# Kernel tuning notes

Hardware: AMD Instinct MI355X
Metric: run time of the kernel (lower is better)

The kernel has to match this reference:

```python
import jax, jax.numpy as jnp
import numpy as np

B, S, W = 64, 128, 20
VOCAB, E, H = 256, 64, 256


def setup_inputs() -> dict:
    key = jax.random.key(0)
    ks = jax.random.split(key, 10)
    return {
        "chars": jax.random.randint(ks[0], (B, S, W), 0, VOCAB),
        "emb": jax.random.uniform(ks[1], (VOCAB, E), jnp.float32, -0.32, 0.32),
        "w1": jax.random.normal(ks[2], (H, E, 1), jnp.float32) * 0.1,
        "b1": jax.random.normal(ks[3], (H,), jnp.float32) * 0.1,
        "w3": jax.random.normal(ks[4], (H, E, 3), jnp.float32) * 0.1,
        "b3": jax.random.normal(ks[5], (H,), jnp.float32) * 0.1,
        "w5": jax.random.normal(ks[6], (H, E, 5), jnp.float32) * 0.1,
        "b5": jax.random.normal(ks[7], (H,), jnp.float32) * 0.1,
        "lw": jax.random.normal(ks[8], (H, 3 * H), jnp.float32) * 0.05,
        "lb": jax.random.normal(ks[9], (H,), jnp.float32) * 0.05,
    }


def _conv_relu_maxpool(x, w, b):
    # x: [N, E, W], w: [H, E, k] ('same' padding k//2) -> [N, H]
    k = w.shape[-1]
    pad = k // 2
    y = jax.lax.conv_general_dilated(
        x, w, window_strides=(1,), padding=[(pad, pad)],
        dimension_numbers=("NCH", "OIH", "NCH"))
    y = jax.nn.relu(y + b[None, :, None])
    return jnp.max(y, axis=2)  # global max over char positions


def reference(chars, emb, w1, b1, w3, b3, w5, b5, lw, lb):
    b, s, wlen = chars.shape
    flat = chars.reshape(-1, wlen)                 # [N, W]
    x = emb[flat]                                  # [N, W, E]
    x = jnp.transpose(x, (0, 2, 1))                # [N, E, W]
    outs = jnp.concatenate([
        _conv_relu_maxpool(x, w1, b1),
        _conv_relu_maxpool(x, w3, b3),
        _conv_relu_maxpool(x, w5, b5),
    ], axis=1)                                     # [N, 3H]
    out = outs @ lw.T + lb                         # [N, H]
    return out.reshape(b, s, -1)
```

## Files before the change

### kernel.cpp

```cpp
#include <hip/hip_runtime.h>
#include <hip/hip_bf16.h>

#define WW 20
#define NW 8192
#define VOCAB 256
#define EE 64
#define HH 256
#define K3 768
#define UNIT 2304

typedef short bf16x8 __attribute__((ext_vector_type(8)));
typedef float f32x4  __attribute__((ext_vector_type(4)));

__device__ __forceinline__ ushort f2bs(float x) {
    __hip_bfloat16 h = __float2bfloat16(x);
    union { __hip_bfloat16 h; ushort u; } c; c.h = h; return c.u;
}
__device__ __forceinline__ float blo(unsigned u) {
    union { unsigned i; float f; } c; c.i = u << 16; return c.f;
}
__device__ __forceinline__ float bhi(unsigned u) {
    union { unsigned i; float f; } c; c.i = u & 0xffff0000u; return c.f;
}
__device__ __forceinline__ unsigned pack2(float lo, float hi) {
    return (unsigned)f2bs(lo) | ((unsigned)f2bs(hi) << 16);
}

#define STEP(j, qq, t8v, a3, a5, mm1, mm3, mm5) {                        \
    float t0 = blo((qq).x), t1 = bhi((qq).x);                            \
    float t2 = blo((qq).y), t3 = bhi((qq).y);                            \
    float t4 = blo((qq).z), t5 = bhi((qq).z);                            \
    float t6 = blo((qq).w), t7 = bhi((qq).w);                            \
    mm1 = fmaxf(mm1, t0);                                                \
    if ((j) + 1 < WW) a3[((j)+1)%3] = t1;                                \
    a3[(j)%3] += t2;                                                     \
    if ((j) >= 1) { a3[((j)-1)%3] += t3;                                 \
                    mm3 = fmaxf(mm3, a3[((j)-1)%3]); }                   \
    if ((j) + 2 < WW) a5[((j)+2)%5] = t4;                                \
    if ((j) + 1 < WW) a5[((j)+1)%5] += t5;                               \
    a5[(j)%5] += t6;                                                     \
    if ((j) >= 1) a5[((j)-1)%5] += t7;                                   \
    if ((j) >= 2) { a5[((j)-2)%5] += (t8v);                              \
                    mm5 = fmaxf(mm5, a5[((j)-2)%5]); }                   \
}


__global__ __launch_bounds__(256) void prep(
        const float* __restrict__ w1,
        const float* __restrict__ w3,
        const float* __restrict__ w5,
        const float* __restrict__ lw,
        float* __restrict__ wTp,
        ushort* __restrict__ lwb) {
    const int bid = blockIdx.x;
    if (bid < 576) {
        int idx = bid * 256 + threadIdx.x;
        int e = idx / UNIT;
        int j = idx - e * UNIT;
        int s = j / 72, r = j - s * 72;
        int tap, h;
        if (r < 64) { tap = r & 7; h = s*8 + (r >> 3); }
        else        { tap = 8;     h = s*8 + (r - 64); }
        float v;
        if (tap == 0)      v = w1[h*EE + e];
        else if (tap <= 3) v = w3[(h*EE + e)*3 + (tap-1)];
        else               v = w5[(h*EE + e)*5 + (tap-4)];
        wTp[idx] = v;
    } else {
        int i = ((bid - 576) * 256 + threadIdx.x) * 4;
        float4 v = *(const float4*)(lw + i);
        ushort4 o4;
        o4.x = f2bs(v.x); o4.y = f2bs(v.y); o4.z = f2bs(v.z); o4.w = f2bs(v.w);
        *(ushort4*)(lwb + i) = o4;
    }
}

__global__ __launch_bounds__(256) void build_tables(
        const float* __restrict__ emb,
        const float* __restrict__ wTp,
        ushort* __restrict__ P5) {
    __shared__ float emb_s[4][EE];
    const int v0 = blockIdx.x * 4;
    const int j  = blockIdx.y * 256 + threadIdx.x;
    const int t  = threadIdx.x;
    emb_s[t >> 6][t & 63] = emb[v0*EE + t];
    __syncthreads();

    float a0 = 0.f, a1 = 0.f, a2 = 0.f, a3 = 0.f;
    const float* wp = wTp + j;
    #pragma unroll 8
    for (int e = 0; e < EE; ++e) {
        float w = wp[e * UNIT];
        a0 += emb_s[0][e] * w; a1 += emb_s[1][e] * w;
        a2 += emb_s[2][e] * w; a3 += emb_s[3][e] * w;
    }
    P5[(size_t)(v0+0)*UNIT + j] = f2bs(a0);
    P5[(size_t)(v0+1)*UNIT + j] = f2bs(a1);
    P5[(size_t)(v0+2)*UNIT + j] = f2bs(a2);
    P5[(size_t)(v0+3)*UNIT + j] = f2bs(a3);
}

__global__ __launch_bounds__(256) void conv_pool(
        const int* __restrict__ chars,
        const ushort* __restrict__ P5,
        const float* __restrict__ b1,
        const float* __restrict__ b3,
        const float* __restrict__ b5,
        ushort* __restrict__ outs) {
    __shared__ uint4 tileq[2304];
    __shared__ int   chs[128*WW];
    const int t = threadIdx.x;
    const int g = blockIdx.x;
    const int s = blockIdx.y;

    {
        const char* src = (const char*)P5 + (size_t)s * 144;
        char* dst = (char*)tileq;
        #pragma unroll
        for (int i = 0; i < 9; ++i) {
            int c = i*256 + t;
            int v = c / 9, k = c - 9*v;
            *(uint4*)(dst + v*144 + k*16) =
                *(const uint4*)(src + (size_t)v*4608 + k*16);
        }
        const int* cg = chars + g * 128 * WW;
        #pragma unroll
        for (int i = 0; i < 10; ++i) chs[i*256 + t] = cg[i*256 + t];
    }
    __syncthreads();

    const int p   = t & 3;
    const int wl0 = t >> 2;
    const char* tile = (const char*)tileq;
    const int h0  = s*8 + p*2;
    const float2 bb1 = *(const float2*)(b1 + h0);
    const float2 bb3 = *(const float2*)(b3 + h0);
    const float2 bb5 = *(const float2*)(b5 + h0);

    #pragma unroll
    for (int cc = 0; cc < 2; ++cc) {
        const int wl = cc*64 + wl0;
        const int n  = g*128 + wl;
        const int* cw = &chs[wl*WW];

        float a3[2][3], a5[2][5], m1[2], m3[2], m5[2];
        #pragma unroll
        for (int i = 0; i < 2; ++i) {
            a3[i][0] = 0.f; a5[i][0] = 0.f; a5[i][1] = 0.f;
            m1[i] = -1e30f; m3[i] = -1e30f; m5[i] = -1e30f;
        }

        uint4 qa[2], qb[2]; unsigned t8[2];
        {
            int c0 = cw[0];
            qa[0] = *(const uint4*)(tile + c0*144 + p*32);
            qb[0] = *(const uint4*)(tile + c0*144 + p*32 + 16);
            t8[0] = *(const unsigned*)(tile + c0*144 + 128 + p*4);
        }

        #pragma unroll
        for (int j = 0; j < WW; ++j) {
            const int cur = j & 1, nxt = cur ^ 1;
            if (j + 1 < WW) {
                int cn = cw[j+1];
                qa[nxt] = *(const uint4*)(tile + cn*144 + p*32);
                qb[nxt] = *(const uint4*)(tile + cn*144 + p*32 + 16);
                t8[nxt] = *(const unsigned*)(tile + cn*144 + 128 + p*4);
            }
            float t8lo = blo(t8[cur]), t8hi = bhi(t8[cur]);
            STEP(j, qa[cur], t8lo, a3[0], a5[0], m1[0], m3[0], m5[0]);
            STEP(j, qb[cur], t8hi, a3[1], a5[1], m1[1], m3[1], m5[1]);
        }
        #pragma unroll
        for (int i = 0; i < 2; ++i) {
            m3[i] = fmaxf(m3[i], a3[i][(WW-1)%3]);
            m5[i] = fmaxf(m5[i], a5[i][(WW-2)%5]);
            m5[i] = fmaxf(m5[i], a5[i][(WW-1)%5]);
        }

        unsigned* op = (unsigned*)(outs + (size_t)n * K3 + h0);
        op[0*(HH/2)] = pack2(fmaxf(m1[0]+bb1.x, 0.f), fmaxf(m1[1]+bb1.y, 0.f));
        op[1*(HH/2)] = pack2(fmaxf(m3[0]+bb3.x, 0.f), fmaxf(m3[1]+bb3.y, 0.f));
        op[2*(HH/2)] = pack2(fmaxf(m5[0]+bb5.x, 0.f), fmaxf(m5[1]+bb5.y, 0.f));
    }
}

__global__ __launch_bounds__(64) void gemm_out(
        const ushort* __restrict__ outs,
        const ushort* __restrict__ lwb,
        const float* __restrict__ lb,
        float* __restrict__ out) {
    const int lane = threadIdx.x;
    const int m0 = blockIdx.x * 32;
    const int n0 = blockIdx.y * 32;
    const int mrow = lane & 15, quad = lane >> 4;

    f32x4 acc00 = (f32x4){0,0,0,0}, acc01 = (f32x4){0,0,0,0};
    f32x4 acc10 = (f32x4){0,0,0,0}, acc11 = (f32x4){0,0,0,0};
    const ushort* ap = outs + (size_t)(m0 + mrow) * K3 + quad * 8;
    const ushort* bp = lwb  + (size_t)(n0 + mrow) * K3 + quad * 8;

    bf16x8 a0 = *(const bf16x8*)ap, a1 = *(const bf16x8*)(ap + 16*K3);
    bf16x8 b0 = *(const bf16x8*)bp, b1 = *(const bf16x8*)(bp + 16*K3);

    #pragma unroll
    for (int it = 0; it < K3/32; ++it) {
        const int kn = (it + 1 < K3/32) ? (it + 1) * 32 : 0;
        bf16x8 a0n = *(const bf16x8*)(ap + kn);
        bf16x8 a1n = *(const bf16x8*)(ap + 16*K3 + kn);
        bf16x8 b0n = *(const bf16x8*)(bp + kn);
        bf16x8 b1n = *(const bf16x8*)(bp + 16*K3 + kn);
        acc00 = __builtin_amdgcn_mfma_f32_16x16x32_bf16(a0, b0, acc00, 0, 0, 0);
        acc01 = __builtin_amdgcn_mfma_f32_16x16x32_bf16(a0, b1, acc01, 0, 0, 0);
        acc10 = __builtin_amdgcn_mfma_f32_16x16x32_bf16(a1, b0, acc10, 0, 0, 0);
        acc11 = __builtin_amdgcn_mfma_f32_16x16x32_bf16(a1, b1, acc11, 0, 0, 0);
        a0 = a0n; a1 = a1n; b0 = b0n; b1 = b1n;
    }

    #pragma unroll
    for (int i = 0; i < 2; ++i) {
        #pragma unroll
        for (int jn = 0; jn < 2; ++jn) {
            const f32x4 acc = (i==0) ? (jn==0 ? acc00 : acc01)
                                     : (jn==0 ? acc10 : acc11);
            int ncol = n0 + jn*16 + mrow;
            float lbv = lb[ncol];
            #pragma unroll
            for (int r = 0; r < 4; ++r)
                out[(size_t)(m0 + i*16 + quad*4 + r)*HH + ncol] = acc[r] + lbv;
        }
    }
}

extern "C" void kernel_launch(void* const* d_in, const int* in_sizes, int n_in,
                              void* d_out, int out_size, void* d_ws, size_t ws_size,
                              hipStream_t stream) {
    const int*   chars = (const int*)d_in[0];
    const float* emb   = (const float*)d_in[1];
    const float* w1    = (const float*)d_in[2];
    const float* b1    = (const float*)d_in[3];
    const float* w3    = (const float*)d_in[4];
    const float* b3    = (const float*)d_in[5];
    const float* w5    = (const float*)d_in[6];
    const float* b5    = (const float*)d_in[7];
    const float* lw    = (const float*)d_in[8];
    const float* lb    = (const float*)d_in[9];

    ushort* P5   = (ushort*)d_ws;
    float*  wTp  = (float*)(P5 + VOCAB * UNIT);
    ushort* outs = (ushort*)(wTp + EE * UNIT);
    ushort* lwb  = outs + (size_t)NW * K3;

    prep<<<768, 256, 0, stream>>>(w1, w3, w5, lw, wTp, lwb);
    build_tables<<<dim3(VOCAB/4, 9), 256, 0, stream>>>(emb, wTp, P5);
    conv_pool<<<dim3(NW/128, 32), 256, 0, stream>>>(chars, P5, b1, b3, b5, outs);
    gemm_out<<<dim3(NW/32, HH/32), 64, 0, stream>>>(outs, lwb, lb, (float*)d_out);
}
```

Measured before the change: 132.9 us.

## Store per-vocab conv tables in fp32 and halve channels per block

The precomputed per-character conv tap table moves from bf16 to fp32, so the conv/pool inner loop no longer unpacks bf16 pairs. Each block now covers 4 output channels instead of 8, so the grid doubles along the channel axis and the shared tile keeps the same byte size. Each thread handles one word with two channels, and the word's character indices are loaded straight into registers instead of staged through shared memory. The cost is double the table traffic from global memory and twice as many blocks, each reloading its tile and reading chars again.

```diff
diff --git a/kernel.cpp b/kernel.cpp
--- a/kernel.cpp
+++ b/kernel.cpp
@@ -7,7 +7,7 @@
 #define EE 64
 #define HH 256
 #define K3 768
-#define UNIT 2304
+#define UNITF 2304
 
 typedef short bf16x8 __attribute__((ext_vector_type(8)));
 typedef float f32x4  __attribute__((ext_vector_type(4)));
@@ -16,30 +16,20 @@
     __hip_bfloat16 h = __float2bfloat16(x);
     union { __hip_bfloat16 h; ushort u; } c; c.h = h; return c.u;
 }
-__device__ __forceinline__ float blo(unsigned u) {
-    union { unsigned i; float f; } c; c.i = u << 16; return c.f;
-}
-__device__ __forceinline__ float bhi(unsigned u) {
-    union { unsigned i; float f; } c; c.i = u & 0xffff0000u; return c.f;
-}
 __device__ __forceinline__ unsigned pack2(float lo, float hi) {
     return (unsigned)f2bs(lo) | ((unsigned)f2bs(hi) << 16);
 }
 
-#define STEP(j, qq, t8v, a3, a5, mm1, mm3, mm5) {                        \
-    float t0 = blo((qq).x), t1 = bhi((qq).x);                            \
-    float t2 = blo((qq).y), t3 = bhi((qq).y);                            \
-    float t4 = blo((qq).z), t5 = bhi((qq).z);                            \
-    float t6 = blo((qq).w), t7 = bhi((qq).w);                            \
-    mm1 = fmaxf(mm1, t0);                                                \
-    if ((j) + 1 < WW) a3[((j)+1)%3] = t1;                                \
-    a3[(j)%3] += t2;                                                     \
-    if ((j) >= 1) { a3[((j)-1)%3] += t3;                                 \
+#define STEPF(j, qa, qb, t8v, a3, a5, mm1, mm3, mm5) {                   \
+    mm1 = fmaxf(mm1, (qa).x);                                            \
+    if ((j) + 1 < WW) a3[((j)+1)%3] = (qa).y;                            \
+    a3[(j)%3] += (qa).z;                                                 \
+    if ((j) >= 1) { a3[((j)-1)%3] += (qa).w;                             \
                     mm3 = fmaxf(mm3, a3[((j)-1)%3]); }                   \
-    if ((j) + 2 < WW) a5[((j)+2)%5] = t4;                                \
-    if ((j) + 1 < WW) a5[((j)+1)%5] += t5;                               \
-    a5[(j)%5] += t6;                                                     \
-    if ((j) >= 1) a5[((j)-1)%5] += t7;                                   \
+    if ((j) + 2 < WW) a5[((j)+2)%5] = (qb).x;                            \
+    if ((j) + 1 < WW) a5[((j)+1)%5] += (qb).y;                           \
+    a5[(j)%5] += (qb).z;                                                 \
+    if ((j) >= 1) a5[((j)-1)%5] += (qb).w;                               \
     if ((j) >= 2) { a5[((j)-2)%5] += (t8v);                              \
                     mm5 = fmaxf(mm5, a5[((j)-2)%5]); }                   \
 }
@@ -55,12 +45,12 @@
     const int bid = blockIdx.x;
     if (bid < 576) {
         int idx = bid * 256 + threadIdx.x;
-        int e = idx / UNIT;
-        int j = idx - e * UNIT;
-        int s = j / 72, r = j - s * 72;
+        int e = idx / UNITF;
+        int j = idx - e * UNITF;
+        int s = j / 36, r = j - s * 36;
         int tap, h;
-        if (r < 64) { tap = r & 7; h = s*8 + (r >> 3); }
-        else        { tap = 8;     h = s*8 + (r - 64); }
+        if (r < 32) { tap = r & 7; h = s*4 + (r >> 3); }
+        else        { tap = 8;     h = s*4 + (r - 32); }
         float v;
         if (tap == 0)      v = w1[h*EE + e];
         else if (tap <= 3) v = w3[(h*EE + e)*3 + (tap-1)];
@@ -78,7 +68,7 @@
 __global__ __launch_bounds__(256) void build_tables(
         const float* __restrict__ emb,
         const float* __restrict__ wTp,
-        ushort* __restrict__ P5) {
+        float* __restrict__ P5f) {
     __shared__ float emb_s[4][EE];
     const int v0 = blockIdx.x * 4;
     const int j  = blockIdx.y * 256 + threadIdx.x;
@@ -90,99 +80,104 @@
     const float* wp = wTp + j;
     #pragma unroll 8
     for (int e = 0; e < EE; ++e) {
-        float w = wp[e * UNIT];
+        float w = wp[e * UNITF];
         a0 += emb_s[0][e] * w; a1 += emb_s[1][e] * w;
         a2 += emb_s[2][e] * w; a3 += emb_s[3][e] * w;
     }
-    P5[(size_t)(v0+0)*UNIT + j] = f2bs(a0);
-    P5[(size_t)(v0+1)*UNIT + j] = f2bs(a1);
-    P5[(size_t)(v0+2)*UNIT + j] = f2bs(a2);
-    P5[(size_t)(v0+3)*UNIT + j] = f2bs(a3);
+    P5f[(size_t)(v0+0)*UNITF + j] = a0;
+    P5f[(size_t)(v0+1)*UNITF + j] = a1;
+    P5f[(size_t)(v0+2)*UNITF + j] = a2;
+    P5f[(size_t)(v0+3)*UNITF + j] = a3;
 }
 
 __global__ __launch_bounds__(256) void conv_pool(
         const int* __restrict__ chars,
-        const ushort* __restrict__ P5,
+        const float* __restrict__ P5f,
         const float* __restrict__ b1,
         const float* __restrict__ b3,
         const float* __restrict__ b5,
         ushort* __restrict__ outs) {
     __shared__ uint4 tileq[2304];
-    __shared__ int   chs[128*WW];
     const int t = threadIdx.x;
     const int g = blockIdx.x;
     const int s = blockIdx.y;
 
     {
-        const char* src = (const char*)P5 + (size_t)s * 144;
+        const char* src = (const char*)(P5f + s * 36);
         char* dst = (char*)tileq;
         #pragma unroll
         for (int i = 0; i < 9; ++i) {
             int c = i*256 + t;
             int v = c / 9, k = c - 9*v;
             *(uint4*)(dst + v*144 + k*16) =
-                *(const uint4*)(src + (size_t)v*4608 + k*16);
-        }
-        const int* cg = chars + g * 128 * WW;
+                *(const uint4*)(src + (size_t)v*9216 + k*16);
+        }
+    }
+
+    const int p  = t & 1;
+    const int wl = t >> 1;
+    const int n  = g*128 + wl;
+    const int h0 = s*4 + p*2;
+
+    int cw[WW];
+    {
+        const int4* cp = (const int4*)(chars + n * WW);
         #pragma unroll
-        for (int i = 0; i < 10; ++i) chs[i*256 + t] = cg[i*256 + t];
-    }
-    __syncthreads();
-
-    const int p   = t & 3;
-    const int wl0 = t >> 2;
-    const char* tile = (const char*)tileq;
-    const int h0  = s*8 + p*2;
+        for (int i = 0; i < 5; ++i) {
+            int4 v = cp[i];
+            cw[i*4+0] = v.x; cw[i*4+1] = v.y; cw[i*4+2] = v.z; cw[i*4+3] = v.w;
+        }
+    }
+
     const float2 bb1 = *(const float2*)(b1 + h0);
     const float2 bb3 = *(const float2*)(b3 + h0);
     const float2 bb5 = *(const float2*)(b5 + h0);
 
-    #pragma unroll
-    for (int cc = 0; cc < 2; ++cc) {
-        const int wl = cc*64 + wl0;
-        const int n  = g*128 + wl;
-        const int* cw = &chs[wl*WW];
-
-        float a3[2][3], a5[2][5], m1[2], m3[2], m5[2];
-        #pragma unroll
-        for (int i = 0; i < 2; ++i) {
-            a3[i][0] = 0.f; a5[i][0] = 0.f; a5[i][1] = 0.f;
-            m1[i] = -1e30f; m3[i] = -1e30f; m5[i] = -1e30f;
-        }
-
-        uint4 qa[2], qb[2]; unsigned t8[2];
-        {
-            int c0 = cw[0];
-            qa[0] = *(const uint4*)(tile + c0*144 + p*32);
-            qb[0] = *(const uint4*)(tile + c0*144 + p*32 + 16);
-            t8[0] = *(const unsigned*)(tile + c0*144 + 128 + p*4);
-        }
-
-        #pragma unroll
-        for (int j = 0; j < WW; ++j) {
-            const int cur = j & 1, nxt = cur ^ 1;
-            if (j + 1 < WW) {
-                int cn = cw[j+1];
-                qa[nxt] = *(const uint4*)(tile + cn*144 + p*32);
-                qb[nxt] = *(const uint4*)(tile + cn*144 + p*32 + 16);
-                t8[nxt] = *(const unsigned*)(tile + cn*144 + 128 + p*4);
-            }
-            float t8lo = blo(t8[cur]), t8hi = bhi(t8[cur]);
-            STEP(j, qa[cur], t8lo, a3[0], a5[0], m1[0], m3[0], m5[0]);
-            STEP(j, qb[cur], t8hi, a3[1], a5[1], m1[1], m3[1], m5[1]);
-        }
-        #pragma unroll
-        for (int i = 0; i < 2; ++i) {
-            m3[i] = fmaxf(m3[i], a3[i][(WW-1)%3]);
-            m5[i] = fmaxf(m5[i], a5[i][(WW-2)%5]);
-            m5[i] = fmaxf(m5[i], a5[i][(WW-1)%5]);
-        }
-
-        unsigned* op = (unsigned*)(outs + (size_t)n * K3 + h0);
-        op[0*(HH/2)] = pack2(fmaxf(m1[0]+bb1.x, 0.f), fmaxf(m1[1]+bb1.y, 0.f));
-        op[1*(HH/2)] = pack2(fmaxf(m3[0]+bb3.x, 0.f), fmaxf(m3[1]+bb3.y, 0.f));
-        op[2*(HH/2)] = pack2(fmaxf(m5[0]+bb5.x, 0.f), fmaxf(m5[1]+bb5.y, 0.f));
-    }
+    __syncthreads();
+    const char* tile = (const char*)tileq;
+
+    float a3[2][3], a5[2][5], m1[2], m3[2], m5[2];
+    #pragma unroll
+    for (int i = 0; i < 2; ++i) {
+        a3[i][0] = 0.f; a5[i][0] = 0.f; a5[i][1] = 0.f;
+        m1[i] = -1e30f; m3[i] = -1e30f; m5[i] = -1e30f;
+    }
+
+    float4 qa0[2], qa1[2], qb0[2], qb1[2]; float2 t8[2];
+    {
+        const char* pc = tile + cw[0]*144 + p*64;
+        qa0[0] = *(const float4*)(pc);
+        qa1[0] = *(const float4*)(pc + 16);
+        qb0[0] = *(const float4*)(pc + 32);
+        qb1[0] = *(const float4*)(pc + 48);
+        t8[0]  = *(const float2*)(tile + cw[0]*144 + 128 + p*8);
+    }
+
+    #pragma unroll
+    for (int j = 0; j < WW; ++j) {
+        const int cur = j & 1, nxt = cur ^ 1;
+        if (j + 1 < WW) {
+            const char* pc = tile + cw[j+1]*144 + p*64;
+            qa0[nxt] = *(const float4*)(pc);
+            qa1[nxt] = *(const float4*)(pc + 16);
+            qb0[nxt] = *(const float4*)(pc + 32);
+            qb1[nxt] = *(const float4*)(pc + 48);
+            t8[nxt]  = *(const float2*)(tile + cw[j+1]*144 + 128 + p*8);
+        }
+        STEPF(j, qa0[cur], qa1[cur], t8[cur].x, a3[0], a5[0], m1[0], m3[0], m5[0]);
+        STEPF(j, qb0[cur], qb1[cur], t8[cur].y, a3[1], a5[1], m1[1], m3[1], m5[1]);
+    }
+    #pragma unroll
+    for (int i = 0; i < 2; ++i) {
+        m3[i] = fmaxf(m3[i], a3[i][(WW-1)%3]);
+        m5[i] = fmaxf(m5[i], a5[i][(WW-2)%5]);
+        m5[i] = fmaxf(m5[i], a5[i][(WW-1)%5]);
+    }
+
+    unsigned* op = (unsigned*)(outs + (size_t)n * K3 + h0);
+    op[0*(HH/2)] = pack2(fmaxf(m1[0]+bb1.x, 0.f), fmaxf(m1[1]+bb1.y, 0.f));
+    op[1*(HH/2)] = pack2(fmaxf(m3[0]+bb3.x, 0.f), fmaxf(m3[1]+bb3.y, 0.f));
+    op[2*(HH/2)] = pack2(fmaxf(m5[0]+bb5.x, 0.f), fmaxf(m5[1]+bb5.y, 0.f));
 }
 
 __global__ __launch_bounds__(64) void gemm_out(
@@ -246,13 +241,13 @@
     const float* lw    = (const float*)d_in[8];
     const float* lb    = (const float*)d_in[9];
 
-    ushort* P5   = (ushort*)d_ws;
-    float*  wTp  = (float*)(P5 + VOCAB * UNIT);
-    ushort* outs = (ushort*)(wTp + EE * UNIT);
+    float*  P5f  = (float*)d_ws;
+    float*  wTp  = P5f + VOCAB * UNITF;
+    ushort* outs = (ushort*)(wTp + EE * UNITF);
     ushort* lwb  = outs + (size_t)NW * K3;
 
     prep<<<768, 256, 0, stream>>>(w1, w3, w5, lw, wTp, lwb);
-    build_tables<<<dim3(VOCAB/4, 9), 256, 0, stream>>>(emb, wTp, P5);
-    conv_pool<<<dim3(NW/128, 32), 256, 0, stream>>>(chars, P5, b1, b3, b5, outs);
+    build_tables<<<dim3(VOCAB/4, 9), 256, 0, stream>>>(emb, wTp, P5f);
+    conv_pool<<<dim3(NW/128, 64), 256, 0, stream>>>(chars, P5f, b1, b3, b5, outs);
     gemm_out<<<dim3(NW/32, HH/32), 64, 0, stream>>>(outs, lwb, lb, (float*)d_out);
 }
```

Result: slower. 144.4 us (+8.6%).
